# Performance work log

Hardware: AMD Instinct MI355X
Metric: run time of the kernel (lower is better)

The kernel has to match this reference:

```python
import jax, jax.numpy as jnp
import numpy as np

H = 256        # h_dim
H2 = 128       # h_dim // 2
S = 512        # sentence_size
G = 64         # number of component graphs in the batched graph
NN = 100000    # total nodes in batched graph
NE = 200000    # total edges
NENT = 20000   # num entities
NREL = 500     # num relations
B = 32         # batch of query timestamps
SEQ = 10       # seq_len


def setup_inputs() -> dict:
    key = jax.random.key(0)
    ks = jax.random.split(key, 32)
    d = {}
    d["node_ids"] = jax.random.randint(ks[0], (NN,), 0, NENT, dtype=jnp.int32)
    d["edge_src"] = jax.random.randint(ks[1], (NE,), 0, NN, dtype=jnp.int32)
    d["edge_dst"] = jax.random.randint(ks[2], (NE,), 0, NN, dtype=jnp.int32)
    d["edge_type"] = jax.random.randint(ks[3], (NE,), 0, NREL, dtype=jnp.int32)
    d["node2graph"] = jnp.sort(jax.random.randint(ks[4], (NN,), 0, G, dtype=jnp.int32))
    d["edge2graph"] = jnp.sort(jax.random.randint(ks[5], (NE,), 0, G, dtype=jnp.int32))
    d["text_emb"] = jax.random.normal(ks[6], (NE, S), dtype=jnp.float32)
    d["time_idx"] = jax.random.randint(ks[7], (B, SEQ), 0, G, dtype=jnp.int32)
    d["len_non_zero"] = jnp.maximum(jax.random.randint(ks[8], (B,), 0, SEQ, dtype=jnp.int32), 1)
    d["ent_embeds"] = jax.random.normal(ks[9], (NENT, 2 * H), dtype=jnp.float32) * 0.05
    d["ent_memory"] = jax.random.normal(ks[10], (NENT, H), dtype=jnp.float32) * 0.05
    d["rel_embeds"] = jax.random.normal(ks[11], (NREL, 2 * H), dtype=jnp.float32) * 0.05
    d["rel_memory"] = jax.random.normal(ks[12], (NREL, H), dtype=jnp.float32) * 0.05
    sc = lambda k, sh: jax.random.normal(k, sh, dtype=jnp.float32) * (1.0 / np.sqrt(sh[0]))
    d["w_node_W"] = sc(ks[13], (3 * H, H)); d["w_node_b"] = jnp.zeros((H,), jnp.float32)
    d["w_rel_W"] = sc(ks[14], (3 * H, H)); d["w_rel_b"] = jnp.zeros((H,), jnp.float32)
    # CompGCN layer 1: H -> H2 (nodes and edges), text S -> H2
    d["Wn1"] = sc(ks[15], (H, H2)); d["Wl1"] = sc(ks[16], (H, H2))
    d["Wt1"] = sc(ks[17], (S, H2)); d["Wr1"] = sc(ks[18], (H, H2))
    d["b1"] = jnp.zeros((H2,), jnp.float32)
    # CompGCN layer 2: H2 -> H, text S -> H
    d["Wn2"] = sc(ks[19], (H2, H)); d["Wl2"] = sc(ks[20], (H2, H))
    d["Wt2"] = sc(ks[21], (S, H)); d["Wr2"] = sc(ks[22], (H2, H))
    d["b2"] = jnp.zeros((H,), jnp.float32)
    return d


def _compgcn_layer(h, e, text, src, dst, Wn, Wl, Wt, Wr, b, n_nodes):
    # composition = subtraction: msg = (h_src - e_h) @ Wn + text @ Wt
    msg = (h[src] - e) @ Wn + text @ Wt                      # [NE, out]
    agg = jax.ops.segment_sum(msg, dst, num_segments=n_nodes)
    deg = jax.ops.segment_sum(jnp.ones((msg.shape[0],), msg.dtype), dst, num_segments=n_nodes)
    agg = agg / jnp.maximum(deg, 1.0)[:, None]
    h_new = jax.nn.relu(agg + h @ Wl + b)                    # self-loop + bias + relu
    e_new = jax.nn.relu(e @ Wr)                              # relation transform
    return h_new, e_new


def reference(node_ids, edge_src, edge_dst, edge_type, node2graph, edge2graph,
              text_emb, time_idx, len_non_zero,
              ent_embeds, ent_memory, rel_embeds, rel_memory,
              w_node_W, w_node_b, w_rel_W, w_rel_b,
              Wn1, Wl1, Wt1, Wr1, b1, Wn2, Wl2, Wt2, Wr2, b2):
    n_nodes = node_ids.shape[0]
    # initial node / edge features: cat(embed[2h], memory[h]) -> Linear(3h, h)
    h = jnp.concatenate([ent_embeds[node_ids], ent_memory[node_ids]], axis=1) @ w_node_W + w_node_b
    e = jnp.concatenate([rel_embeds[edge_type], rel_memory[edge_type]], axis=1) @ w_rel_W + w_rel_b
    # two CompGCN relational message-passing layers: H -> H2 -> H
    h, e = _compgcn_layer(h, e, text_emb, edge_src, edge_dst, Wn1, Wl1, Wt1, Wr1, b1, n_nodes)
    h, e = _compgcn_layer(h, e, text_emb, edge_src, edge_dst, Wn2, Wl2, Wt2, Wr2, b2, n_nodes)
    # dgl.max_nodes / dgl.max_edges: per-graph max pooling (maxpool == 1)
    gn = jax.ops.segment_max(h, node2graph, num_segments=G)   # [G, H]
    ge = jax.ops.segment_max(e, edge2graph, num_segments=G)   # [G, H]
    global_info = jnp.concatenate([gn, ge], axis=-1)          # [G, 2H]
    # ragged temporal gather: embed_seq[i, j] = global_info[time_to_idx[time_list[i][j]]]
    seq = global_info[time_idx]                               # [B, SEQ, 2H]
    mask = (jnp.arange(SEQ, dtype=jnp.int32)[None, :] < len_non_zero[:, None])
    seq = seq * mask[..., None].astype(seq.dtype)             # zeros past len_non_zero
    # dropout at eval time is identity
    return seq, len_non_zero
```

## Files before the change

kernel.cpp:

```cpp
#include <hip/hip_runtime.h>

#define HD    256
#define HD2   128
#define SDIM  512
#define GNUM  64
#define NN    100000
#define NE    200000
#define NENT  20000
#define NREL  500
#define BNUM  32
#define SEQL  10

typedef __attribute__((ext_vector_type(4))) float f32x4;
typedef __attribute__((ext_vector_type(8))) short bf16x8;

__device__ __forceinline__ short to_bf(float f) {
    unsigned u = __float_as_uint(f);
    u += 0x7fff + ((u >> 16) & 1);
    return (short)(u >> 16);
}
__device__ __forceinline__ float bf_to_f(unsigned short u) {
    return __uint_as_float(((unsigned)u) << 16);
}


__global__ void k_cnt(const int* __restrict__ edst, int* __restrict__ cnt) {
    int e = blockIdx.x * 256 + threadIdx.x;
    if (e < NE) atomicAdd(&cnt[edst[e]], 1);
}

__global__ void k_scan_blk(const int* __restrict__ cnt, int* __restrict__ row_off,
                           int* __restrict__ bsum) {
    __shared__ int s[256];
    int i = blockIdx.x * 256 + threadIdx.x;
    int v = cnt[i];
    s[threadIdx.x] = v;
    __syncthreads();
    for (int d = 1; d < 256; d <<= 1) {
        int t = (threadIdx.x >= d) ? s[threadIdx.x - d] : 0;
        __syncthreads();
        s[threadIdx.x] += t;
        __syncthreads();
    }
    row_off[i] = s[threadIdx.x] - v;
    if (threadIdx.x == 255) bsum[blockIdx.x] = s[255];
}

__global__ void k_scan_top(int* __restrict__ bsum) {
    __shared__ int s[512];
    int v = (threadIdx.x < 391) ? bsum[threadIdx.x] : 0;
    s[threadIdx.x] = v;
    __syncthreads();
    for (int d = 1; d < 512; d <<= 1) {
        int t = (threadIdx.x >= d) ? s[threadIdx.x - d] : 0;
        __syncthreads();
        s[threadIdx.x] += t;
        __syncthreads();
    }
    if (threadIdx.x < 391) bsum[threadIdx.x] = s[threadIdx.x] - v;
}

__global__ void k_scan_add(int* __restrict__ row_off, const int* __restrict__ bsum,
                           int* __restrict__ cur) {
    int i = blockIdx.x * 256 + threadIdx.x;
    int v = row_off[i] + bsum[blockIdx.x];
    row_off[i] = v;
    cur[i] = v;
}

__global__ void k_fill(const int* __restrict__ edst, const int* __restrict__ esrc,
                       const int* __restrict__ etype, const int* __restrict__ node_ids,
                       int* __restrict__ cur, int* __restrict__ eidx,
                       int* __restrict__ esrcC, int* __restrict__ etC,
                       int* __restrict__ nidC) {
    int e = blockIdx.x * 256 + threadIdx.x;
    if (e < NE) {
        int pos = atomicAdd(&cur[edst[e]], 1);
        int s = esrc[e];
        eidx[pos] = e;
        esrcC[pos] = s;
        etC[pos] = etype[e];
        nidC[pos] = node_ids[s];
    }
}


__global__ void k_rel_feat(const float* __restrict__ rel_emb, const float* __restrict__ rel_mem,
                           const float* __restrict__ W, const float* __restrict__ b,
                           float* __restrict__ rel_feat) {
    __shared__ float s[768];
    int r = blockIdx.x, j = threadIdx.x;
    for (int k = j; k < 768; k += 256)
        s[k] = (k < 512) ? rel_emb[r * 512 + k] : rel_mem[r * 256 + (k - 512)];
    __syncthreads();
    float acc = b[j];
    for (int k = 0; k < 768; ++k) acc += s[k] * W[k * 256 + j];
    rel_feat[r * 256 + j] = acc;
}

__global__ void k_rel_l1(const float* __restrict__ rel_feat, const float* __restrict__ Wn1,
                         const float* __restrict__ Wr1, float* __restrict__ ecomb,
                         float* __restrict__ er1) {
    __shared__ float s[256];
    int r = blockIdx.x, j = threadIdx.x;
    s[j] = rel_feat[r * 256 + j];
    __syncthreads();
    if (j < 128) {
        float acc = 0.f;
        for (int k = 0; k < 256; ++k) acc += s[k] * Wn1[k * 128 + j];
        ecomb[r * 384 + j] = acc;
    } else {
        int jj = j - 128;
        float acc = 0.f;
        for (int k = 0; k < 256; ++k) acc += s[k] * Wr1[k * 128 + jj];
        er1[r * 128 + jj] = fmaxf(acc, 0.f);
    }
}

__global__ void k_rel_l2(const float* __restrict__ er1, const float* __restrict__ Wr2,
                         const float* __restrict__ Wn2, float* __restrict__ er2,
                         float* __restrict__ ecomb) {
    __shared__ float s[128];
    int r = blockIdx.x, j = threadIdx.x;
    if (j < 128) s[j] = er1[r * 128 + j];
    __syncthreads();
    float a = 0.f, c = 0.f;
    for (int k = 0; k < 128; ++k) {
        float v = s[k];
        a += v * Wr2[k * 256 + j];
        c += v * Wn2[k * 256 + j];
    }
    er2[r * 256 + j] = fmaxf(a, 0.f);
    ecomb[r * 384 + 128 + j] = c;
}


__global__ void k_cw(const float* __restrict__ wnW, const float* __restrict__ Wn1,
                     const float* __restrict__ Wl1, float* __restrict__ cw) {
    __shared__ float s[256];
    int k = blockIdx.x, j = threadIdx.x;
    s[j] = wnW[k * 256 + j];
    __syncthreads();
    float acc = 0.f;
    if (j < 128) {
        for (int m = 0; m < 256; ++m) acc += s[m] * Wn1[m * 128 + j];
    } else {
        int jj = j - 128;
        for (int m = 0; m < 256; ++m) acc += s[m] * Wl1[m * 128 + jj];
    }
    cw[k * 256 + j] = acc;
}

__global__ void k_cb(const float* __restrict__ wnb, const float* __restrict__ Wn1,
                     const float* __restrict__ Wl1, float* __restrict__ bc) {
    int j = threadIdx.x;
    float acc = 0.f;
    if (j < 128) {
        for (int m = 0; m < 256; ++m) acc += wnb[m] * Wn1[m * 128 + j];
    } else {
        int jj = j - 128;
        for (int m = 0; m < 256; ++m) acc += wnb[m] * Wl1[m * 128 + jj];
    }
    bc[j] = acc;
}

__global__ void k_pack(const float* __restrict__ src, bf16x8* __restrict__ dst,
                       int K, int N) {
    int KF = K >> 5;
    int fid = blockIdx.x;
    int n = fid / KF, kk = fid - n * KF;
    int lane = threadIdx.x;
    int col = n * 16 + (lane & 15);
    int kb = kk * 32 + (lane >> 4) * 8;
    bf16x8 v;
#pragma unroll
    for (int j = 0; j < 8; ++j) v[j] = to_bf(src[(size_t)(kb + j) * N + col]);
    dst[(size_t)fid * 64 + lane] = v;
}


__global__ void __launch_bounds__(256) k_ent(const float* __restrict__ ee,
                                             const float* __restrict__ em,
                                             const bf16x8* __restrict__ cwf,
                                             const float* __restrict__ bc,
                                             float* __restrict__ ha1,
                                             float* __restrict__ hb1) {
    __shared__ bf16x8 sA[2048];
    int tid = threadIdx.x;
    int e0 = blockIdx.x * 64;
    int wave = tid >> 6, lane = tid & 63;
    int gs = (tid >> 4) & 3, rs = tid & 15;
    int rowS = ((tid >> 6) & 3) * 16 + rs;
    int ent = e0 + rowS;
    if (ent >= NENT) ent = NENT - 1;
    f32x4 acc[4][4];
#pragma unroll
    for (int mf = 0; mf < 4; ++mf)
#pragma unroll
        for (int nf = 0; nf < 4; ++nf) acc[mf][nf] = (f32x4)0.f;

    for (int ch = 0; ch < 3; ++ch) {
        if (ch) __syncthreads();
#pragma unroll
        for (int it = 0; it < 8; ++it) {
            int gc = ch * 256 + it * 32 + gs * 8;
            const float4* p = (gc < 512)
                ? (const float4*)(ee + (size_t)ent * 512 + gc)
                : (const float4*)(em + (size_t)ent * 256 + (gc - 512));
            float4 x = p[0], y = p[1];
            bf16x8 v;
            v[0] = to_bf(x.x); v[1] = to_bf(x.y); v[2] = to_bf(x.z); v[3] = to_bf(x.w);
            v[4] = to_bf(y.x); v[5] = to_bf(y.y); v[6] = to_bf(y.z); v[7] = to_bf(y.w);
            sA[it * 256 + tid] = v;
        }
        __syncthreads();
#pragma unroll
        for (int kkl = 0; kkl < 8; ++kkl) {
            bf16x8 a[4], b[4];
#pragma unroll
            for (int mf = 0; mf < 4; ++mf) a[mf] = sA[kkl * 256 + mf * 64 + lane];
#pragma unroll
            for (int nf = 0; nf < 4; ++nf)
                b[nf] = cwf[(size_t)((wave * 4 + nf) * 24 + ch * 8 + kkl) * 64 + lane];
#pragma unroll
            for (int mf = 0; mf < 4; ++mf)
#pragma unroll
                for (int nf = 0; nf < 4; ++nf)
                    acc[mf][nf] = __builtin_amdgcn_mfma_f32_16x16x32_bf16(a[mf], b[nf],
                                                                          acc[mf][nf], 0, 0, 0);
        }
    }
    int gq = lane >> 4, cl = lane & 15;
#pragma unroll
    for (int mf = 0; mf < 4; ++mf)
#pragma unroll
        for (int nf = 0; nf < 4; ++nf) {
            int c = wave * 64 + nf * 16 + cl;
            float bb = bc[c];
#pragma unroll
            for (int q = 0; q < 4; ++q) {
                int m = e0 + mf * 16 + gq * 4 + q;
                if (m < NENT) {
                    float val = acc[mf][nf][q] + bb;
                    if (c < 128) ha1[(size_t)m * 128 + c] = val;
                    else hb1[(size_t)m * 128 + (c - 128)] = val;
                }
            }
        }
}


__global__ void __launch_bounds__(256, 2) k_edge(const float* __restrict__ text,
                                                 const bf16x8* __restrict__ wtf,
                                                 unsigned short* __restrict__ msg) {
    __shared__ bf16x8 sA[4096];
    int tid = threadIdx.x;
    size_t e0 = (size_t)blockIdx.x * 64;
    int R = ((tid >> 6) << 4) + (tid & 15);
    int g = (tid >> 4) & 3;
    const float* trow = text + (e0 + R) * 512 + g * 8;

    float4 xv[16], yv[16];
#pragma unroll
    for (int kk = 0; kk < 16; ++kk) {
        const float4* p = (const float4*)(trow + kk * 32);
        xv[kk] = p[0];
        yv[kk] = p[1];
    }
#pragma unroll
    for (int kk = 0; kk < 16; ++kk) {
        bf16x8 v;
        v[0] = to_bf(xv[kk].x); v[1] = to_bf(xv[kk].y);
        v[2] = to_bf(xv[kk].z); v[3] = to_bf(xv[kk].w);
        v[4] = to_bf(yv[kk].x); v[5] = to_bf(yv[kk].y);
        v[6] = to_bf(yv[kk].z); v[7] = to_bf(yv[kk].w);
        sA[kk * 256 + tid] = v;
    }
    __syncthreads();

    int wave = tid >> 6, lane = tid & 63;
    f32x4 acc[4][6];
#pragma unroll
    for (int mf = 0; mf < 4; ++mf)
#pragma unroll
        for (int nf = 0; nf < 6; ++nf) acc[mf][nf] = (f32x4)0.f;

#pragma unroll
    for (int kk = 0; kk < 16; ++kk) {
        bf16x8 a[4], b[6];
#pragma unroll
        for (int mf = 0; mf < 4; ++mf) a[mf] = sA[kk * 256 + mf * 64 + lane];
#pragma unroll
        for (int nf = 0; nf < 6; ++nf)
            b[nf] = wtf[(size_t)((wave * 6 + nf) * 16 + kk) * 64 + lane];
#pragma unroll
        for (int mf = 0; mf < 4; ++mf)
#pragma unroll
            for (int nf = 0; nf < 6; ++nf)
                acc[mf][nf] = __builtin_amdgcn_mfma_f32_16x16x32_bf16(a[mf], b[nf],
                                                                      acc[mf][nf], 0, 0, 0);
    }

    int gq = lane >> 4, cl = lane & 15;
#pragma unroll
    for (int mf = 0; mf < 4; ++mf)
#pragma unroll
        for (int nf = 0; nf < 6; ++nf) {
            int c = wave * 96 + nf * 16 + cl;
            f32x4 v = acc[mf][nf];
#pragma unroll
            for (int q = 0; q < 4; ++q) {
                int row = mf * 16 + gq * 4 + q;
                msg[(e0 + row) * 384 + c] = (unsigned short)to_bf(v[q]);
            }
        }
}


__global__ void __launch_bounds__(256) k_agg(const unsigned short* __restrict__ msg,
                                             const int* __restrict__ row_off,
                                             const int* __restrict__ eidx,
                                             const int* __restrict__ etC,
                                             const int* __restrict__ nidC,
                                             const int* __restrict__ node_ids,
                                             const float* __restrict__ ha1,
                                             const float* __restrict__ ecomb,
                                             const float* __restrict__ hb1,
                                             const float* __restrict__ b1,
                                             float* __restrict__ h1,
                                             float* __restrict__ agg2) {
    int n = blockIdx.x * 4 + (threadIdx.x >> 6);
    int lane = threadIdx.x & 63;
    if (n >= NN) return;
    int beg = row_off[n], end = row_off[n + 1];
    float d = fmaxf((float)(end - beg), 1.f);
    int nid0 = node_ids[n];
    int c = lane * 2;
    float a0 = 0.f, a1 = 0.f, a2 = 0.f, a3 = 0.f, a4 = 0.f, a5 = 0.f;
    const unsigned* m32 = (const unsigned*)msg;
    for (int i = beg; i < end; ++i) {
        size_t e = (size_t)eidx[i];
        int et = etC[i], nid = nidC[i];
        size_t base = e * 192;
        unsigned u0 = m32[base + lane];
        unsigned u1 = m32[base + 64 + lane];
        unsigned u2 = m32[base + 128 + lane];
        const float2 ec0 = *(const float2*)(ecomb + (size_t)et * 384 + c);
        const float2 ec1 = *(const float2*)(ecomb + (size_t)et * 384 + 128 + c);
        const float2 ec2 = *(const float2*)(ecomb + (size_t)et * 384 + 256 + c);
        const float2 hv = *(const float2*)(ha1 + (size_t)nid * 128 + c);
        a0 += bf_to_f((unsigned short)(u0 & 0xffff)) + hv.x - ec0.x;
        a1 += bf_to_f((unsigned short)(u0 >> 16)) + hv.y - ec0.y;
        a2 += bf_to_f((unsigned short)(u1 & 0xffff)) - ec1.x;
        a3 += bf_to_f((unsigned short)(u1 >> 16)) - ec1.y;
        a4 += bf_to_f((unsigned short)(u2 & 0xffff)) - ec2.x;
        a5 += bf_to_f((unsigned short)(u2 >> 16)) - ec2.y;
    }
    const float2 hb = *(const float2*)(hb1 + (size_t)nid0 * 128 + c);
    const float2 bb = *(const float2*)(b1 + c);
    float2 hvo;
    hvo.x = fmaxf(a0 / d + hb.x + bb.x, 0.f);
    hvo.y = fmaxf(a1 / d + hb.y + bb.y, 0.f);
    *(float2*)(h1 + (size_t)n * 128 + c) = hvo;
    float2 g0; g0.x = a2; g0.y = a3;
    float2 g1; g1.x = a4; g1.y = a5;
    *(float2*)(agg2 + (size_t)n * 256 + c) = g0;
    *(float2*)(agg2 + (size_t)n * 256 + 128 + c) = g1;
}


__global__ void __launch_bounds__(256) k_s1(const float* __restrict__ h1,
                                            const int* __restrict__ row_off,
                                            const int* __restrict__ esrcC,
                                            float* __restrict__ s1) {
    int n = blockIdx.x * 4 + (threadIdx.x >> 6);
    int lane = threadIdx.x & 63;
    if (n >= NN) return;
    int beg = row_off[n], end = row_off[n + 1];
    float2 acc; acc.x = 0.f; acc.y = 0.f;
    for (int i = beg; i < end; ++i) {
        int src = esrcC[i];
        float2 v = ((const float2*)(h1 + (size_t)src * 128))[lane];
        acc.x += v.x; acc.y += v.y;
    }
    ((float2*)(s1 + (size_t)n * 128))[lane] = acc;
}


__global__ void __launch_bounds__(256) k_h2(const float* __restrict__ s1,
                                            const float* __restrict__ h1,
                                            const float* __restrict__ agg2,
                                            const int* __restrict__ cnt,
                                            const bf16x8* __restrict__ wn2f,
                                            const bf16x8* __restrict__ wl2f,
                                            const float* __restrict__ b2,
                                            float* __restrict__ h2) {
    __shared__ bf16x8 sS[1024], sH[1024];
    int tid = threadIdx.x, n0 = blockIdx.x * 64;
    int wave = tid >> 6, lane = tid & 63;
    {
        int gsv = (tid >> 4) & 3, rsv = tid & 15;
        int row = ((tid >> 6) & 3) * 16 + rsv;
        int m = n0 + row;
        if (m >= NN) m = NN - 1;
#pragma unroll
        for (int kk = 0; kk < 4; ++kk) {
            int cb = kk * 32 + gsv * 8;
            const float4* ps = (const float4*)(s1 + (size_t)m * 128 + cb);
            const float4* ph = (const float4*)(h1 + (size_t)m * 128 + cb);
            float4 sx = ps[0], sy = ps[1], hx = ph[0], hy = ph[1];
            bf16x8 vs, vh;
            vs[0] = to_bf(sx.x); vs[1] = to_bf(sx.y); vs[2] = to_bf(sx.z); vs[3] = to_bf(sx.w);
            vs[4] = to_bf(sy.x); vs[5] = to_bf(sy.y); vs[6] = to_bf(sy.z); vs[7] = to_bf(sy.w);
            vh[0] = to_bf(hx.x); vh[1] = to_bf(hx.y); vh[2] = to_bf(hx.z); vh[3] = to_bf(hx.w);
            vh[4] = to_bf(hy.x); vh[5] = to_bf(hy.y); vh[6] = to_bf(hy.z); vh[7] = to_bf(hy.w);
            sS[kk * 256 + tid] = vs;
            sH[kk * 256 + tid] = vh;
        }
    }
    __syncthreads();
    f32x4 aa[4][4], ab[4][4];
#pragma unroll
    for (int mf = 0; mf < 4; ++mf)
#pragma unroll
        for (int nf = 0; nf < 4; ++nf) { aa[mf][nf] = (f32x4)0.f; ab[mf][nf] = (f32x4)0.f; }
#pragma unroll
    for (int kk = 0; kk < 4; ++kk) {
        bf16x8 a1[4], a2[4], bv1[4], bv2[4];
#pragma unroll
        for (int mf = 0; mf < 4; ++mf) {
            a1[mf] = sS[kk * 256 + mf * 64 + lane];
            a2[mf] = sH[kk * 256 + mf * 64 + lane];
        }
#pragma unroll
        for (int nf = 0; nf < 4; ++nf) {
            bv1[nf] = wn2f[(size_t)((wave * 4 + nf) * 4 + kk) * 64 + lane];
            bv2[nf] = wl2f[(size_t)((wave * 4 + nf) * 4 + kk) * 64 + lane];
        }
#pragma unroll
        for (int mf = 0; mf < 4; ++mf)
#pragma unroll
            for (int nf = 0; nf < 4; ++nf) {
                aa[mf][nf] = __builtin_amdgcn_mfma_f32_16x16x32_bf16(a1[mf], bv1[nf],
                                                                     aa[mf][nf], 0, 0, 0);
                ab[mf][nf] = __builtin_amdgcn_mfma_f32_16x16x32_bf16(a2[mf], bv2[nf],
                                                                     ab[mf][nf], 0, 0, 0);
            }
    }
    int gq = lane >> 4, cl = lane & 15;
    float dinv[4][4];
#pragma unroll
    for (int mf = 0; mf < 4; ++mf)
#pragma unroll
        for (int q = 0; q < 4; ++q) {
            int m = n0 + mf * 16 + gq * 4 + q;
            if (m >= NN) m = NN - 1;
            dinv[mf][q] = 1.f / fmaxf((float)cnt[m], 1.f);
        }
    float b2v[4];
#pragma unroll
    for (int nf = 0; nf < 4; ++nf) b2v[nf] = b2[wave * 64 + nf * 16 + cl];
#pragma unroll
    for (int mf = 0; mf < 4; ++mf)
#pragma unroll
        for (int nf = 0; nf < 4; ++nf) {
            int c = wave * 64 + nf * 16 + cl;
#pragma unroll
            for (int q = 0; q < 4; ++q) {
                int m = n0 + mf * 16 + gq * 4 + q;
                if (m >= NN) m = NN - 1;
                float araw = agg2[(size_t)m * 256 + c];
                aa[mf][nf][q] = fmaxf((araw + aa[mf][nf][q]) * dinv[mf][q]
                                      + ab[mf][nf][q] + b2v[nf], 0.f);
            }
        }
    __builtin_amdgcn_sched_barrier(0);
#pragma unroll
    for (int mf = 0; mf < 4; ++mf)
#pragma unroll
        for (int nf = 0; nf < 4; ++nf) {
            int c = wave * 64 + nf * 16 + cl;
#pragma unroll
            for (int q = 0; q < 4; ++q) {
                int m = n0 + mf * 16 + gq * 4 + q;
                if (m < NN) h2[(size_t)m * 256 + c] = aa[mf][nf][q];
            }
        }
}


__device__ __forceinline__ int lower_bound_i(const int* __restrict__ a, int n, int v) {
    int lo = 0, hi = n;
    while (lo < hi) {
        int m = (lo + hi) >> 1;
        if (a[m] < v) lo = m + 1; else hi = m;
    }
    return lo;
}

__global__ void k_gmax_nodes(const float* __restrict__ h2, const int* __restrict__ n2g,
                             float* __restrict__ gn) {
    int g = blockIdx.x, q = blockIdx.y, j = threadIdx.x;
    int lo = lower_bound_i(n2g, NN, g);
    int hi = lower_bound_i(n2g, NN, g + 1);
    float mx = 0.f;
    for (int n = lo + q; n < hi; n += 16) mx = fmaxf(mx, h2[(size_t)n * 256 + j]);
    atomicMax((int*)&gn[g * 256 + j], __float_as_int(mx));
}

__global__ void k_gmax_edges(const float* __restrict__ er2, const int* __restrict__ e2g,
                             const int* __restrict__ etype, float* __restrict__ ge) {
    int g = blockIdx.x, q = blockIdx.y, j = threadIdx.x;
    int lo = lower_bound_i(e2g, NE, g);
    int hi = lower_bound_i(e2g, NE, g + 1);
    float mx = 0.f;
    for (int e = lo + q; e < hi; e += 16) mx = fmaxf(mx, er2[etype[e] * 256 + j]);
    atomicMax((int*)&ge[g * 256 + j], __float_as_int(mx));
}

__global__ void k_out(const float* __restrict__ gn, const float* __restrict__ ge,
                      const int* __restrict__ time_idx, const int* __restrict__ lens,
                      float* __restrict__ out) {
    int idx = blockIdx.x * 256 + threadIdx.x;
    const int NOUT = BNUM * SEQL * 512;
    if (idx < NOUT) {
        int j = idx & 511;
        int bt = idx >> 9;
        int b = bt / SEQL, t = bt - b * SEQL;
        float v = 0.f;
        if (t < lens[b]) {
            int g = time_idx[bt];
            v = (j < 256) ? gn[g * 256 + j] : ge[g * 256 + (j - 256)];
        }
        out[idx] = v;
    } else if (idx < NOUT + BNUM) {
        int b = idx - NOUT;
        out[idx] = (float)lens[b];
    }
}


extern "C" void kernel_launch(void* const* d_in, const int* in_sizes, int n_in,
                              void* d_out, int out_size, void* d_ws, size_t ws_size,
                              hipStream_t stream) {
    const int*   node_ids  = (const int*)d_in[0];
    const int*   edge_src  = (const int*)d_in[1];
    const int*   edge_dst  = (const int*)d_in[2];
    const int*   edge_type = (const int*)d_in[3];
    const int*   node2g    = (const int*)d_in[4];
    const int*   edge2g    = (const int*)d_in[5];
    const float* text_emb  = (const float*)d_in[6];
    const int*   time_idx  = (const int*)d_in[7];
    const int*   lens      = (const int*)d_in[8];
    const float* ent_emb   = (const float*)d_in[9];
    const float* ent_mem   = (const float*)d_in[10];
    const float* rel_emb   = (const float*)d_in[11];
    const float* rel_mem   = (const float*)d_in[12];
    const float* w_node_W  = (const float*)d_in[13];
    const float* w_node_b  = (const float*)d_in[14];
    const float* w_rel_W   = (const float*)d_in[15];
    const float* w_rel_b   = (const float*)d_in[16];
    const float* Wn1 = (const float*)d_in[17];
    const float* Wl1 = (const float*)d_in[18];
    const float* Wt1 = (const float*)d_in[19];
    const float* Wr1 = (const float*)d_in[20];
    const float* b1  = (const float*)d_in[21];
    const float* Wn2 = (const float*)d_in[22];
    const float* Wl2 = (const float*)d_in[23];
    const float* Wt2 = (const float*)d_in[24];
    const float* Wr2 = (const float*)d_in[25];
    const float* b2  = (const float*)d_in[26];

    float* ws = (float*)d_ws;
    size_t off = 0;
    float* rel_feat = ws + off; off += (size_t)NREL * 256;
    float* er1      = ws + off; off += (size_t)NREL * 128;
    float* er2      = ws + off; off += (size_t)NREL * 256;
    float* ecomb    = ws + off; off += (size_t)NREL * 384;
    float* ha1      = ws + off; off += (size_t)NENT * 128;
    float* hb1      = ws + off; off += (size_t)NENT * 128;
    float* cw       = ws + off; off += (size_t)768 * 256;
    float* bc       = ws + off; off += 256;
    bf16x8* wtf  = (bf16x8*)(ws + off); off += (size_t)24 * 16 * 64 * 4;
    bf16x8* cwf  = (bf16x8*)(ws + off); off += (size_t)16 * 24 * 64 * 4;
    bf16x8* wn2f = (bf16x8*)(ws + off); off += (size_t)16 * 4 * 64 * 4;
    bf16x8* wl2f = (bf16x8*)(ws + off); off += (size_t)16 * 4 * 64 * 4;
    int*   cnt = (int*)(ws + off);
    size_t zoff = off;          off += 100096;
    float* gn  = ws + off;      off += (size_t)GNUM * 256;
    float* ge  = ws + off;      off += (size_t)GNUM * 256;
    size_t zbytes = (off - zoff) * sizeof(float);
    int* row_off = (int*)(ws + off); off += 100352;
    int* cur     = (int*)(ws + off); off += 100096;
    int* bsum    = (int*)(ws + off); off += 512;
    int* eidx    = (int*)(ws + off); off += (size_t)NE;
    int* esrcC   = (int*)(ws + off); off += (size_t)NE;
    int* etC     = (int*)(ws + off); off += (size_t)NE;
    int* nidC    = (int*)(ws + off); off += (size_t)NE;
    unsigned short* msg = (unsigned short*)(ws + off);
    float* s1 = ws + off;
    off += (size_t)NE * 384 / 2;
    float* h1   = ws + off; off += (size_t)NN * 128;
    float* agg2 = ws + off; off += (size_t)NN * 256;
    float* h2   = ws + off; off += (size_t)NN * 256;

    hipMemsetAsync((void*)cnt, 0, zbytes, stream);

    k_cnt<<<(NE + 255) / 256, 256, 0, stream>>>(edge_dst, cnt);
    k_scan_blk<<<391, 256, 0, stream>>>(cnt, row_off, bsum);
    k_scan_top<<<1, 512, 0, stream>>>(bsum);
    k_scan_add<<<391, 256, 0, stream>>>(row_off, bsum, cur);
    k_fill<<<(NE + 255) / 256, 256, 0, stream>>>(edge_dst, edge_src, edge_type, node_ids,
                                                 cur, eidx, esrcC, etC, nidC);

    k_rel_feat<<<NREL, 256, 0, stream>>>(rel_emb, rel_mem, w_rel_W, w_rel_b, rel_feat);
    k_rel_l1<<<NREL, 256, 0, stream>>>(rel_feat, Wn1, Wr1, ecomb, er1);
    k_rel_l2<<<NREL, 256, 0, stream>>>(er1, Wr2, Wn2, er2, ecomb);

    k_cw<<<768, 256, 0, stream>>>(w_node_W, Wn1, Wl1, cw);
    k_cb<<<1, 256, 0, stream>>>(w_node_b, Wn1, Wl1, bc);
    k_pack<<<8 * 16, 64, 0, stream>>>(Wt1, wtf, 512, 128);
    k_pack<<<16 * 16, 64, 0, stream>>>(Wt2, wtf + (size_t)8 * 16 * 64, 512, 256);
    k_pack<<<16 * 24, 64, 0, stream>>>(cw, cwf, 768, 256);
    k_pack<<<16 * 4, 64, 0, stream>>>(Wn2, wn2f, 128, 256);
    k_pack<<<16 * 4, 64, 0, stream>>>(Wl2, wl2f, 128, 256);

    k_ent<<<(NENT + 63) / 64, 256, 0, stream>>>(ent_emb, ent_mem, cwf, bc, ha1, hb1);

    k_edge<<<NE / 64, 256, 0, stream>>>(text_emb, wtf, msg);

    k_agg<<<NN / 4, 256, 0, stream>>>(msg, row_off, eidx, etC, nidC, node_ids,
                                      ha1, ecomb, hb1, b1, h1, agg2);
    k_s1<<<NN / 4, 256, 0, stream>>>(h1, row_off, esrcC, s1);
    k_h2<<<(NN + 63) / 64, 256, 0, stream>>>(s1, h1, agg2, cnt, wn2f, wl2f, b2, h2);

    k_gmax_nodes<<<dim3(GNUM, 16), 256, 0, stream>>>(h2, node2g, gn);
    k_gmax_edges<<<dim3(GNUM, 16), 256, 0, stream>>>(er2, edge2g, edge_type, ge);
    k_out<<<(BNUM * SEQL * 512 + BNUM + 255) / 256, 256, 0, stream>>>(gn, ge, time_idx, lens,
                                                                      (float*)d_out);
}
```

Measured before the change: 684.3 us.

## Aggregate raw text per node before projection instead of projecting every edge

Moves the linear text projection after the scatter-sum, so text rows are summed per destination node first and the MFMA GEMM then runs over NN nodes instead of NE edges. This halves the GEMM work and removes the per-edge bf16 message buffer write and read-back. The rest of the per-edge terms (ecomb, ha1) are folded into a separate per-node buffer. It costs a gather of fp32 text rows in the aggregation kernel, an extra fold buffer, and bf16 rounding now applied to summed text instead of per-edge outputs. The workspace is reshuffled so that fold shares memory with h2.

```diff
diff --git a/kernel.cpp b/kernel.cpp
--- a/kernel.cpp
+++ b/kernel.cpp
@@ -18,9 +18,6 @@
     unsigned u = __float_as_uint(f);
     u += 0x7fff + ((u >> 16) & 1);
     return (short)(u >> 16);
-}
-__device__ __forceinline__ float bf_to_f(unsigned short u) {
-    return __uint_as_float(((unsigned)u) << 16);
 }
 
 
@@ -250,122 +247,147 @@
 }
 
 
-__global__ void __launch_bounds__(256, 2) k_edge(const float* __restrict__ text,
-                                                 const bf16x8* __restrict__ wtf,
-                                                 unsigned short* __restrict__ msg) {
-    __shared__ bf16x8 sA[4096];
-    int tid = threadIdx.x;
-    size_t e0 = (size_t)blockIdx.x * 64;
-    int R = ((tid >> 6) << 4) + (tid & 15);
-    int g = (tid >> 4) & 3;
-    const float* trow = text + (e0 + R) * 512 + g * 8;
-
-    float4 xv[16], yv[16];
-#pragma unroll
-    for (int kk = 0; kk < 16; ++kk) {
-        const float4* p = (const float4*)(trow + kk * 32);
-        xv[kk] = p[0];
-        yv[kk] = p[1];
-    }
-#pragma unroll
-    for (int kk = 0; kk < 16; ++kk) {
-        bf16x8 v;
-        v[0] = to_bf(xv[kk].x); v[1] = to_bf(xv[kk].y);
-        v[2] = to_bf(xv[kk].z); v[3] = to_bf(xv[kk].w);
-        v[4] = to_bf(yv[kk].x); v[5] = to_bf(yv[kk].y);
-        v[6] = to_bf(yv[kk].z); v[7] = to_bf(yv[kk].w);
-        sA[kk * 256 + tid] = v;
-    }
-    __syncthreads();
-
-    int wave = tid >> 6, lane = tid & 63;
-    f32x4 acc[4][6];
-#pragma unroll
-    for (int mf = 0; mf < 4; ++mf)
-#pragma unroll
-        for (int nf = 0; nf < 6; ++nf) acc[mf][nf] = (f32x4)0.f;
-
-#pragma unroll
-    for (int kk = 0; kk < 16; ++kk) {
-        bf16x8 a[4], b[6];
-#pragma unroll
-        for (int mf = 0; mf < 4; ++mf) a[mf] = sA[kk * 256 + mf * 64 + lane];
-#pragma unroll
-        for (int nf = 0; nf < 6; ++nf)
-            b[nf] = wtf[(size_t)((wave * 6 + nf) * 16 + kk) * 64 + lane];
-#pragma unroll
-        for (int mf = 0; mf < 4; ++mf)
-#pragma unroll
-            for (int nf = 0; nf < 6; ++nf)
-                acc[mf][nf] = __builtin_amdgcn_mfma_f32_16x16x32_bf16(a[mf], b[nf],
-                                                                      acc[mf][nf], 0, 0, 0);
-    }
-
-    int gq = lane >> 4, cl = lane & 15;
-#pragma unroll
-    for (int mf = 0; mf < 4; ++mf)
-#pragma unroll
-        for (int nf = 0; nf < 6; ++nf) {
-            int c = wave * 96 + nf * 16 + cl;
-            f32x4 v = acc[mf][nf];
-#pragma unroll
-            for (int q = 0; q < 4; ++q) {
-                int row = mf * 16 + gq * 4 + q;
-                msg[(e0 + row) * 384 + c] = (unsigned short)to_bf(v[q]);
-            }
-        }
-}
-
-
-__global__ void __launch_bounds__(256) k_agg(const unsigned short* __restrict__ msg,
-                                             const int* __restrict__ row_off,
-                                             const int* __restrict__ eidx,
-                                             const int* __restrict__ etC,
-                                             const int* __restrict__ nidC,
-                                             const int* __restrict__ node_ids,
-                                             const float* __restrict__ ha1,
-                                             const float* __restrict__ ecomb,
-                                             const float* __restrict__ hb1,
-                                             const float* __restrict__ b1,
-                                             float* __restrict__ h1,
-                                             float* __restrict__ agg2) {
+__global__ void __launch_bounds__(256) k_tsum(const float* __restrict__ text,
+                                              const int* __restrict__ row_off,
+                                              const int* __restrict__ eidx,
+                                              const int* __restrict__ etC,
+                                              const int* __restrict__ nidC,
+                                              const float* __restrict__ ha1,
+                                              const float* __restrict__ ecomb,
+                                              unsigned short* __restrict__ tsumb,
+                                              float* __restrict__ fold) {
     int n = blockIdx.x * 4 + (threadIdx.x >> 6);
     int lane = threadIdx.x & 63;
     if (n >= NN) return;
     int beg = row_off[n], end = row_off[n + 1];
-    float d = fmaxf((float)(end - beg), 1.f);
-    int nid0 = node_ids[n];
     int c = lane * 2;
-    float a0 = 0.f, a1 = 0.f, a2 = 0.f, a3 = 0.f, a4 = 0.f, a5 = 0.f;
-    const unsigned* m32 = (const unsigned*)msg;
+    f32x4 t0 = (f32x4)0.f, t1 = (f32x4)0.f;
+    float f0 = 0.f, f1 = 0.f, f2 = 0.f, f3 = 0.f, f4 = 0.f, f5 = 0.f;
+    float h0 = 0.f, h1v = 0.f;
     for (int i = beg; i < end; ++i) {
-        size_t e = (size_t)eidx[i];
+        const float* tr = text + (size_t)eidx[i] * 512 + lane * 8;
+        t0 += *(const f32x4*)tr;
+        t1 += *(const f32x4*)(tr + 4);
         int et = etC[i], nid = nidC[i];
-        size_t base = e * 192;
-        unsigned u0 = m32[base + lane];
-        unsigned u1 = m32[base + 64 + lane];
-        unsigned u2 = m32[base + 128 + lane];
-        const float2 ec0 = *(const float2*)(ecomb + (size_t)et * 384 + c);
-        const float2 ec1 = *(const float2*)(ecomb + (size_t)et * 384 + 128 + c);
-        const float2 ec2 = *(const float2*)(ecomb + (size_t)et * 384 + 256 + c);
+        const float2 e0 = *(const float2*)(ecomb + (size_t)et * 384 + c);
+        const float2 e1 = *(const float2*)(ecomb + (size_t)et * 384 + 128 + c);
+        const float2 e2 = *(const float2*)(ecomb + (size_t)et * 384 + 256 + c);
         const float2 hv = *(const float2*)(ha1 + (size_t)nid * 128 + c);
-        a0 += bf_to_f((unsigned short)(u0 & 0xffff)) + hv.x - ec0.x;
-        a1 += bf_to_f((unsigned short)(u0 >> 16)) + hv.y - ec0.y;
-        a2 += bf_to_f((unsigned short)(u1 & 0xffff)) - ec1.x;
-        a3 += bf_to_f((unsigned short)(u1 >> 16)) - ec1.y;
-        a4 += bf_to_f((unsigned short)(u2 & 0xffff)) - ec2.x;
-        a5 += bf_to_f((unsigned short)(u2 >> 16)) - ec2.y;
-    }
-    const float2 hb = *(const float2*)(hb1 + (size_t)nid0 * 128 + c);
-    const float2 bb = *(const float2*)(b1 + c);
-    float2 hvo;
-    hvo.x = fmaxf(a0 / d + hb.x + bb.x, 0.f);
-    hvo.y = fmaxf(a1 / d + hb.y + bb.y, 0.f);
-    *(float2*)(h1 + (size_t)n * 128 + c) = hvo;
-    float2 g0; g0.x = a2; g0.y = a3;
-    float2 g1; g1.x = a4; g1.y = a5;
-    *(float2*)(agg2 + (size_t)n * 256 + c) = g0;
-    *(float2*)(agg2 + (size_t)n * 256 + 128 + c) = g1;
+        f0 -= e0.x; f1 -= e0.y;
+        f2 -= e1.x; f3 -= e1.y;
+        f4 -= e2.x; f5 -= e2.y;
+        h0 += hv.x; h1v += hv.y;
+    }
+    bf16x8 tb;
+    tb[0] = to_bf(t0[0]); tb[1] = to_bf(t0[1]); tb[2] = to_bf(t0[2]); tb[3] = to_bf(t0[3]);
+    tb[4] = to_bf(t1[0]); tb[5] = to_bf(t1[1]); tb[6] = to_bf(t1[2]); tb[7] = to_bf(t1[3]);
+    *(bf16x8*)(tsumb + (size_t)n * 512 + lane * 8) = tb;
+    float2 w0; w0.x = f0 + h0; w0.y = f1 + h1v;
+    float2 w1; w1.x = f2; w1.y = f3;
+    float2 w2; w2.x = f4; w2.y = f5;
+    *(float2*)(fold + (size_t)n * 384 + c) = w0;
+    *(float2*)(fold + (size_t)n * 384 + 128 + c) = w1;
+    *(float2*)(fold + (size_t)n * 384 + 256 + c) = w2;
+}
+
+
+__global__ void __launch_bounds__(256, 2) k_node(const unsigned short* __restrict__ tsumb,
+                                                 const float* __restrict__ fold,
+                                                 const int* __restrict__ node_ids,
+                                                 const int* __restrict__ cnt,
+                                                 const bf16x8* __restrict__ wtf,
+                                                 const float* __restrict__ hb1,
+                                                 const float* __restrict__ b1,
+                                                 float* __restrict__ h1,
+                                                 float* __restrict__ agg2) {
+    __shared__ bf16x8 sA[4096];
+    __shared__ int s_nid[64];
+    int tid = threadIdx.x;
+    int n0 = blockIdx.x * 64;
+    if (tid < 64) {
+        int m = n0 + tid;
+        if (m >= NN) m = NN - 1;
+        s_nid[tid] = node_ids[m];
+    }
+    int R = ((tid >> 6) << 4) + (tid & 15);
+    int g = (tid >> 4) & 3;
+    int rowm = n0 + R;
+    if (rowm >= NN) rowm = NN - 1;
+    const unsigned short* trow = tsumb + (size_t)rowm * 512 + g * 8;
+    bf16x8 rv[16];
+#pragma unroll
+    for (int kk = 0; kk < 16; ++kk) rv[kk] = *(const bf16x8*)(trow + kk * 32);
+#pragma unroll
+    for (int kk = 0; kk < 16; ++kk) sA[kk * 256 + tid] = rv[kk];
+    __syncthreads();
+
+    int wave = tid >> 6, lane = tid & 63;
+    f32x4 acc[4][6];
+#pragma unroll
+    for (int mf = 0; mf < 4; ++mf)
+#pragma unroll
+        for (int nf = 0; nf < 6; ++nf) acc[mf][nf] = (f32x4)0.f;
+
+#pragma unroll
+    for (int kk = 0; kk < 16; ++kk) {
+        bf16x8 a[4], b[6];
+#pragma unroll
+        for (int mf = 0; mf < 4; ++mf) a[mf] = sA[kk * 256 + mf * 64 + lane];
+#pragma unroll
+        for (int nf = 0; nf < 6; ++nf)
+            b[nf] = wtf[(size_t)((wave * 6 + nf) * 16 + kk) * 64 + lane];
+#pragma unroll
+        for (int mf = 0; mf < 4; ++mf)
+#pragma unroll
+            for (int nf = 0; nf < 6; ++nf)
+                acc[mf][nf] = __builtin_amdgcn_mfma_f32_16x16x32_bf16(a[mf], b[nf],
+                                                                      acc[mf][nf], 0, 0, 0);
+    }
+
+    int gq = lane >> 4, cl = lane & 15;
+    float dinv[4][4];
+#pragma unroll
+    for (int mf = 0; mf < 4; ++mf)
+#pragma unroll
+        for (int q = 0; q < 4; ++q) {
+            int m = n0 + mf * 16 + gq * 4 + q;
+            if (m >= NN) m = NN - 1;
+            dinv[mf][q] = 1.f / fmaxf((float)cnt[m], 1.f);
+        }
+#pragma unroll
+    for (int mf = 0; mf < 4; ++mf)
+#pragma unroll
+        for (int nf = 0; nf < 6; ++nf) {
+            int c = wave * 96 + nf * 16 + cl;
+            float bb = (c < 128) ? b1[c] : 0.f;
+#pragma unroll
+            for (int q = 0; q < 4; ++q) {
+                int row = mf * 16 + gq * 4 + q;
+                int m = n0 + row;
+                if (m >= NN) m = NN - 1;
+                float v = acc[mf][nf][q] + fold[(size_t)m * 384 + c];
+                if (c < 128) {
+                    int nid = s_nid[row];
+                    v = fmaxf(v * dinv[mf][q] + hb1[(size_t)nid * 128 + c] + bb, 0.f);
+                }
+                acc[mf][nf][q] = v;
+            }
+        }
+    __builtin_amdgcn_sched_barrier(0);
+#pragma unroll
+    for (int mf = 0; mf < 4; ++mf)
+#pragma unroll
+        for (int nf = 0; nf < 6; ++nf) {
+            int c = wave * 96 + nf * 16 + cl;
+#pragma unroll
+            for (int q = 0; q < 4; ++q) {
+                int m = n0 + mf * 16 + gq * 4 + q;
+                if (m < NN) {
+                    if (c < 128) h1[(size_t)m * 128 + c] = acc[mf][nf][q];
+                    else agg2[(size_t)m * 256 + (c - 128)] = acc[mf][nf][q];
+                }
+            }
+        }
 }
 
 
@@ -597,12 +619,14 @@
     int* esrcC   = (int*)(ws + off); off += (size_t)NE;
     int* etC     = (int*)(ws + off); off += (size_t)NE;
     int* nidC    = (int*)(ws + off); off += (size_t)NE;
-    unsigned short* msg = (unsigned short*)(ws + off);
+    unsigned short* tsumb = (unsigned short*)(ws + off);
     float* s1 = ws + off;
-    off += (size_t)NE * 384 / 2;
+    off += (size_t)NN * 512 / 2;
+    float* fold = ws + off;
+    float* h2   = ws + off;
+    off += (size_t)NN * 384;
     float* h1   = ws + off; off += (size_t)NN * 128;
     float* agg2 = ws + off; off += (size_t)NN * 256;
-    float* h2   = ws + off; off += (size_t)NN * 256;
 
     hipMemsetAsync((void*)cnt, 0, zbytes, stream);
 
@@ -627,10 +651,12 @@
 
     k_ent<<<(NENT + 63) / 64, 256, 0, stream>>>(ent_emb, ent_mem, cwf, bc, ha1, hb1);
 
-    k_edge<<<NE / 64, 256, 0, stream>>>(text_emb, wtf, msg);
-
-    k_agg<<<NN / 4, 256, 0, stream>>>(msg, row_off, eidx, etC, nidC, node_ids,
-                                      ha1, ecomb, hb1, b1, h1, agg2);
+    k_tsum<<<NN / 4, 256, 0, stream>>>(text_emb, row_off, eidx, etC, nidC,
+                                       ha1, ecomb, tsumb, fold);
+
+    k_node<<<(NN + 63) / 64, 256, 0, stream>>>(tsumb, fold, node_ids, cnt, wtf,
+                                               hb1, b1, h1, agg2);
+
     k_s1<<<NN / 4, 256, 0, stream>>>(h1, row_off, esrcC, s1);
     k_h2<<<(NN + 63) / 64, 256, 0, stream>>>(s1, h1, agg2, cnt, wn2f, wl2f, b2, h2);
 
```

Result: slower. 895.2 us (+30.8%).

## Store h1/agg2 in bf16 and fuse node max-pooling into k_h2 epilogue

Applied to the files above, without the earlier changes.

Intermediate node features h1 and the layer-2 aggregate agg2 are now written and read as bf16 instead of fp32, halving their memory traffic in k_agg, k_s1 and k_h2. The separate k_gmax_nodes pass is removed. k_h2 now reduces its output tile per graph with wave shuffles and atomicMax straight into gn, so h2 is never written to global memory. In exchange it loses precision on h1 and agg2, and blocks that straddle a graph boundary fall back to per-element atomics.

```diff
diff --git a/kernel.cpp b/kernel.cpp
--- a/kernel.cpp
+++ b/kernel.cpp
@@ -327,8 +327,8 @@
                                              const float* __restrict__ ecomb,
                                              const float* __restrict__ hb1,
                                              const float* __restrict__ b1,
-                                             float* __restrict__ h1,
-                                             float* __restrict__ agg2) {
+                                             unsigned short* __restrict__ h1b,
+                                             unsigned short* __restrict__ agg2b) {
     int n = blockIdx.x * 4 + (threadIdx.x >> 6);
     int lane = threadIdx.x & 63;
     if (n >= NN) return;
@@ -358,18 +358,21 @@
     }
     const float2 hb = *(const float2*)(hb1 + (size_t)nid0 * 128 + c);
     const float2 bb = *(const float2*)(b1 + c);
-    float2 hvo;
-    hvo.x = fmaxf(a0 / d + hb.x + bb.x, 0.f);
-    hvo.y = fmaxf(a1 / d + hb.y + bb.y, 0.f);
-    *(float2*)(h1 + (size_t)n * 128 + c) = hvo;
-    float2 g0; g0.x = a2; g0.y = a3;
-    float2 g1; g1.x = a4; g1.y = a5;
-    *(float2*)(agg2 + (size_t)n * 256 + c) = g0;
-    *(float2*)(agg2 + (size_t)n * 256 + 128 + c) = g1;
-}
-
-
-__global__ void __launch_bounds__(256) k_s1(const float* __restrict__ h1,
+    float hx = fmaxf(a0 / d + hb.x + bb.x, 0.f);
+    float hy = fmaxf(a1 / d + hb.y + bb.y, 0.f);
+    unsigned hp = ((unsigned)(unsigned short)to_bf(hx)) |
+                  (((unsigned)(unsigned short)to_bf(hy)) << 16);
+    ((unsigned*)h1b)[(size_t)n * 64 + lane] = hp;
+    unsigned g0 = ((unsigned)(unsigned short)to_bf(a2)) |
+                  (((unsigned)(unsigned short)to_bf(a3)) << 16);
+    unsigned g1 = ((unsigned)(unsigned short)to_bf(a4)) |
+                  (((unsigned)(unsigned short)to_bf(a5)) << 16);
+    ((unsigned*)agg2b)[(size_t)n * 128 + lane] = g0;
+    ((unsigned*)agg2b)[(size_t)n * 128 + 64 + lane] = g1;
+}
+
+
+__global__ void __launch_bounds__(256) k_s1(const unsigned short* __restrict__ h1b,
                                             const int* __restrict__ row_off,
                                             const int* __restrict__ esrcC,
                                             float* __restrict__ s1) {
@@ -378,26 +381,35 @@
     if (n >= NN) return;
     int beg = row_off[n], end = row_off[n + 1];
     float2 acc; acc.x = 0.f; acc.y = 0.f;
+    const unsigned* h32 = (const unsigned*)h1b;
     for (int i = beg; i < end; ++i) {
         int src = esrcC[i];
-        float2 v = ((const float2*)(h1 + (size_t)src * 128))[lane];
-        acc.x += v.x; acc.y += v.y;
+        unsigned u = h32[(size_t)src * 64 + lane];
+        acc.x += bf_to_f((unsigned short)(u & 0xffff));
+        acc.y += bf_to_f((unsigned short)(u >> 16));
     }
     ((float2*)(s1 + (size_t)n * 128))[lane] = acc;
 }
 
 
 __global__ void __launch_bounds__(256) k_h2(const float* __restrict__ s1,
-                                            const float* __restrict__ h1,
-                                            const float* __restrict__ agg2,
+                                            const unsigned short* __restrict__ h1b,
+                                            const unsigned short* __restrict__ agg2b,
                                             const int* __restrict__ cnt,
+                                            const int* __restrict__ n2g,
                                             const bf16x8* __restrict__ wn2f,
                                             const bf16x8* __restrict__ wl2f,
                                             const float* __restrict__ b2,
-                                            float* __restrict__ h2) {
+                                            float* __restrict__ gn) {
     __shared__ bf16x8 sS[1024], sH[1024];
+    __shared__ int s_g[64];
     int tid = threadIdx.x, n0 = blockIdx.x * 64;
     int wave = tid >> 6, lane = tid & 63;
+    if (tid < 64) {
+        int m = n0 + tid;
+        if (m >= NN) m = NN - 1;
+        s_g[tid] = n2g[m];
+    }
     {
         int gsv = (tid >> 4) & 3, rsv = tid & 15;
         int row = ((tid >> 6) & 3) * 16 + rsv;
@@ -407,13 +419,11 @@
         for (int kk = 0; kk < 4; ++kk) {
             int cb = kk * 32 + gsv * 8;
             const float4* ps = (const float4*)(s1 + (size_t)m * 128 + cb);
-            const float4* ph = (const float4*)(h1 + (size_t)m * 128 + cb);
-            float4 sx = ps[0], sy = ps[1], hx = ph[0], hy = ph[1];
-            bf16x8 vs, vh;
+            float4 sx = ps[0], sy = ps[1];
+            bf16x8 vs;
             vs[0] = to_bf(sx.x); vs[1] = to_bf(sx.y); vs[2] = to_bf(sx.z); vs[3] = to_bf(sx.w);
             vs[4] = to_bf(sy.x); vs[5] = to_bf(sy.y); vs[6] = to_bf(sy.z); vs[7] = to_bf(sy.w);
-            vh[0] = to_bf(hx.x); vh[1] = to_bf(hx.y); vh[2] = to_bf(hx.z); vh[3] = to_bf(hx.w);
-            vh[4] = to_bf(hy.x); vh[5] = to_bf(hy.y); vh[6] = to_bf(hy.z); vh[7] = to_bf(hy.w);
+            bf16x8 vh = *(const bf16x8*)(h1b + (size_t)m * 128 + cb);
             sS[kk * 256 + tid] = vs;
             sH[kk * 256 + tid] = vh;
         }
@@ -469,23 +479,44 @@
             for (int q = 0; q < 4; ++q) {
                 int m = n0 + mf * 16 + gq * 4 + q;
                 if (m >= NN) m = NN - 1;
-                float araw = agg2[(size_t)m * 256 + c];
+                float araw = bf_to_f(agg2b[(size_t)m * 256 + c]);
                 aa[mf][nf][q] = fmaxf((araw + aa[mf][nf][q]) * dinv[mf][q]
                                       + ab[mf][nf][q] + b2v[nf], 0.f);
             }
         }
-    __builtin_amdgcn_sched_barrier(0);
-#pragma unroll
-    for (int mf = 0; mf < 4; ++mf)
+    int g0 = s_g[0], g63 = s_g[63];
+    if (g0 == g63) {
 #pragma unroll
         for (int nf = 0; nf < 4; ++nf) {
-            int c = wave * 64 + nf * 16 + cl;
+            float mx = 0.f;
+#pragma unroll
+            for (int mf = 0; mf < 4; ++mf)
+#pragma unroll
+                for (int q = 0; q < 4; ++q) mx = fmaxf(mx, aa[mf][nf][q]);
+            mx = fmaxf(mx, __shfl_xor(mx, 16));
+            mx = fmaxf(mx, __shfl_xor(mx, 32));
+            if (gq == 0) {
+                int c = wave * 64 + nf * 16 + cl;
+                atomicMax((int*)&gn[(size_t)g0 * 256 + c], __float_as_int(mx));
+            }
+        }
+    } else {
+#pragma unroll
+        for (int mf = 0; mf < 4; ++mf)
 #pragma unroll
             for (int q = 0; q < 4; ++q) {
-                int m = n0 + mf * 16 + gq * 4 + q;
-                if (m < NN) h2[(size_t)m * 256 + c] = aa[mf][nf][q];
+                int row = mf * 16 + gq * 4 + q;
+                int m = n0 + row;
+                if (m >= NN) continue;
+                int gg = s_g[row];
+#pragma unroll
+                for (int nf = 0; nf < 4; ++nf) {
+                    int c = wave * 64 + nf * 16 + cl;
+                    atomicMax((int*)&gn[(size_t)gg * 256 + c],
+                              __float_as_int(aa[mf][nf][q]));
+                }
             }
-        }
+    }
 }
 
 
@@ -496,16 +527,6 @@
         if (a[m] < v) lo = m + 1; else hi = m;
     }
     return lo;
-}
-
-__global__ void k_gmax_nodes(const float* __restrict__ h2, const int* __restrict__ n2g,
-                             float* __restrict__ gn) {
-    int g = blockIdx.x, q = blockIdx.y, j = threadIdx.x;
-    int lo = lower_bound_i(n2g, NN, g);
-    int hi = lower_bound_i(n2g, NN, g + 1);
-    float mx = 0.f;
-    for (int n = lo + q; n < hi; n += 16) mx = fmaxf(mx, h2[(size_t)n * 256 + j]);
-    atomicMax((int*)&gn[g * 256 + j], __float_as_int(mx));
 }
 
 __global__ void k_gmax_edges(const float* __restrict__ er2, const int* __restrict__ e2g,
@@ -600,9 +621,8 @@
     unsigned short* msg = (unsigned short*)(ws + off);
     float* s1 = ws + off;
     off += (size_t)NE * 384 / 2;
-    float* h1   = ws + off; off += (size_t)NN * 128;
-    float* agg2 = ws + off; off += (size_t)NN * 256;
-    float* h2   = ws + off; off += (size_t)NN * 256;
+    unsigned short* h1b   = (unsigned short*)(ws + off); off += (size_t)NN * 64;
+    unsigned short* agg2b = (unsigned short*)(ws + off); off += (size_t)NN * 128;
 
     hipMemsetAsync((void*)cnt, 0, zbytes, stream);
 
@@ -630,11 +650,11 @@
     k_edge<<<NE / 64, 256, 0, stream>>>(text_emb, wtf, msg);
 
     k_agg<<<NN / 4, 256, 0, stream>>>(msg, row_off, eidx, etC, nidC, node_ids,
-                                      ha1, ecomb, hb1, b1, h1, agg2);
-    k_s1<<<NN / 4, 256, 0, stream>>>(h1, row_off, esrcC, s1);
-    k_h2<<<(NN + 63) / 64, 256, 0, stream>>>(s1, h1, agg2, cnt, wn2f, wl2f, b2, h2);
-
-    k_gmax_nodes<<<dim3(GNUM, 16), 256, 0, stream>>>(h2, node2g, gn);
+                                      ha1, ecomb, hb1, b1, h1b, agg2b);
+    k_s1<<<NN / 4, 256, 0, stream>>>(h1b, row_off, esrcC, s1);
+    k_h2<<<(NN + 63) / 64, 256, 0, stream>>>(s1, h1b, agg2b, cnt, node2g,
+                                             wn2f, wl2f, b2, gn);
+
     k_gmax_edges<<<dim3(GNUM, 16), 256, 0, stream>>>(er2, edge2g, edge_type, ge);
     k_out<<<(BNUM * SEQL * 512 + BNUM + 255) / 256, 256, 0, stream>>>(gn, ge, time_idx, lens,
                                                                       (float*)d_out);
```

New measurement: 581.2 us. 1.18x faster.
